# Kernel optimization log

Measured on AMD Instinct MI355X. Metric: run time of the kernel, lower is better.

The kernel has to match this reference:

```python
import jax, jax.numpy as jnp
import numpy as np

B, S, D, H = 2, 2048, 2048, 16
DK = D // H
THETA = 10000.0


def setup_inputs() -> dict:
    key = jax.random.key(0)
    ks = jax.random.split(key, 5)
    scale = 0.02
    return {
        "x": jax.random.normal(ks[0], (B, S, D), dtype=jnp.float32),
        "W_Q": jax.random.normal(ks[1], (D, D), dtype=jnp.float32) * scale,
        "W_K": jax.random.normal(ks[2], (D, D), dtype=jnp.float32) * scale,
        "W_V": jax.random.normal(ks[3], (D, D), dtype=jnp.float32) * scale,
        "W_O": jax.random.normal(ks[4], (D, D), dtype=jnp.float32) * scale,
        "token_positions": jnp.arange(S, dtype=jnp.int32),
    }


def _rope(x, pos):
    # x: [B, S, H, DK]; pos: [S]. Interleaved-pair rotation (cs336 RoPE).
    half = DK // 2
    inv_freq = THETA ** (-(jnp.arange(half, dtype=jnp.float32) / half))  # [half]
    ang = pos.astype(jnp.float32)[:, None] * inv_freq[None, :]           # [S, half]
    cos = jnp.cos(ang)[None, :, None, :]                                 # [1,S,1,half]
    sin = jnp.sin(ang)[None, :, None, :]
    x1, x2 = x[..., ::2], x[..., 1::2]
    r1 = x1 * cos - x2 * sin
    r2 = x1 * sin + x2 * cos
    return jnp.stack([r1, r2], axis=-1).reshape(x.shape)


def reference(x, W_Q, W_K, W_V, W_O, token_positions):
    # QKV projections (Linear with no bias: y = x @ W^T)
    Q = (x @ W_Q.T).reshape(B, S, H, DK)
    K = (x @ W_K.T).reshape(B, S, H, DK)
    V = (x @ W_V.T).reshape(B, S, H, DK)
    Q = _rope(Q, token_positions)
    K = _rope(K, token_positions)
    scores = jnp.einsum("bqhd,bkhd->bhqk", Q, K) / jnp.sqrt(jnp.float32(DK))
    causal = jnp.tril(jnp.ones((S, S), dtype=bool))  # True = attend
    scores = jnp.where(causal[None, None], scores, -jnp.inf)
    attn = jax.nn.softmax(scores, axis=-1)
    out = jnp.einsum("bhqk,bkhd->bqhd", attn, V).reshape(B, S, D)
    return out @ W_O.T
```

## Files before the change

kernel.cpp:

```cpp
#include <hip/hip_runtime.h>
#include <hip/hip_bf16.h>
#include <cstdint>
#include <cstddef>

#define B_ 2
#define S_ 2048
#define D_ 2048
#define H_ 16
#define DK_ 128
#define M_ (B_*S_)

typedef __attribute__((ext_vector_type(8))) __bf16 bf16x8;
typedef __attribute__((ext_vector_type(4))) float f32x4;
typedef __attribute__((ext_vector_type(16))) float f32x16;

__device__ __forceinline__ unsigned short f2bf(float f) {
  union { float f; unsigned int u; } v; v.f = f;
  unsigned int r = (v.u + 0x7fffu + ((v.u >> 16) & 1u)) >> 16;
  return (unsigned short)r;
}
__device__ __forceinline__ float bf2f(unsigned short b) {
  union { unsigned int u; float f; } v; v.u = ((unsigned int)b) << 16;
  return v.f;
}

__device__ __forceinline__ void gld16(const void* g, void* l) {
  __builtin_amdgcn_global_load_lds(
      (const __attribute__((address_space(1))) unsigned int*)g,
      (__attribute__((address_space(3))) unsigned int*)l, 16, 0, 0);
}

__global__ void cvt_all(const float* __restrict__ x,  const float* __restrict__ Wq,
                        const float* __restrict__ Wk, const float* __restrict__ Wv,
                        const float* __restrict__ Wo, unsigned short* __restrict__ dst) {
  size_t i = ((size_t)blockIdx.x * blockDim.x + threadIdx.x) * 4;
  const float* src;
  size_t off;
  if (i < ((size_t)M_ * D_)) {
    src = x; off = i;
  } else {
    size_t j = i - (size_t)M_ * D_;
    int w = (int)(j >> 22);
    off = j & ((1u << 22) - 1);
    src = (w == 0) ? Wq : (w == 1) ? Wk : (w == 2) ? Wv : Wo;
  }
  float4 v = *(const float4*)(src + off);
  dst[i+0] = f2bf(v.x); dst[i+1] = f2bf(v.y);
  dst[i+2] = f2bf(v.z); dst[i+3] = f2bf(v.w);
}

__global__ __launch_bounds__(512, 2) void gemm_qkv(const unsigned short* __restrict__ A,
                                                   const unsigned short* __restrict__ W0,
                                                   const unsigned short* __restrict__ W1,
                                                   const unsigned short* __restrict__ W2,
                                                   unsigned short* __restrict__ C0,
                                                   unsigned short* __restrict__ C1,
                                                   unsigned short* __restrict__ C2,
                                                   int M, int N, int K) {
  __shared__ unsigned short sA[2][2][256 * 32];
  __shared__ unsigned short sB[2][2][256 * 32];
  const int id   = blockIdx.x;
  const int tid  = threadIdx.x;
  const int lane = tid & 63;
  const int wid  = tid >> 6;
  const int l16 = lane & 15, quad = lane >> 4;
  const int col16 = quad ^ ((lane >> 1) & 3);
  const int qk_log = (lane & 3) ^ ((lane >> 3) & 3);
  const int srow = lane >> 2;
  const int NT = K >> 6;

  if (id < 256) {
    const int z = id >> 7, r = id & 127;
    const unsigned short* Bt = z ? W1 : W0;
    unsigned short* Cout = z ? C1 : C0;
    const int bm = (r >> 3) * 256, bn = (r & 7) * 256;
    const int wm = wid >> 2, wn = wid & 3;

    f32x4 acc[8][4];
    #pragma unroll
    for (int i = 0; i < 8; ++i)
      #pragma unroll
      for (int j = 0; j < 4; ++j)
        acc[i][j] = (f32x4){0.f, 0.f, 0.f, 0.f};

    auto stage = [&](const unsigned short* __restrict__ g, int rowbase,
                     unsigned short* l, int t, int kh) {
      const unsigned short* src = g + (size_t)rowbase * K + t * 64 + kh * 32 + qk_log * 8;
      #pragma unroll
      for (int p = 0; p < 2; ++p) {
        const int i = wid * 2 + p;
        gld16(src + (size_t)(i * 16 + srow) * K, l + i * 512);
      }
    };

    stage(A,  bm, &sA[0][0][0], 0, 0);
    stage(Bt, bn, &sB[0][0][0], 0, 0);
    stage(A,  bm, &sA[0][1][0], 0, 1);
    stage(Bt, bn, &sB[0][1][0], 0, 1);
    stage(A,  bm, &sA[1][0][0], 1, 0);
    stage(Bt, bn, &sB[1][0][0], 1, 0);
    asm volatile("s_waitcnt vmcnt(4)" ::: "memory");
    __builtin_amdgcn_s_barrier();

    for (int t = 0; t < NT; ++t) {
      const int buf = t & 1;
      bf16x8 bfrag[4];
      #pragma unroll
      for (int ph = 0; ph < 4; ++ph) {
        const int ks = ph >> 1;
        const int mh = ph & 1;
        bf16x8 afrag[4];
        const unsigned short* aP = &sA[buf][ks][0] +
            (size_t)((wm * 128 + mh * 64 + l16) * 4 + col16) * 8;
        #pragma unroll
        for (int mf = 0; mf < 4; ++mf)
          afrag[mf] = *(const bf16x8*)(aP + mf * 512);
        if (mh == 0) {
          const unsigned short* bP = &sB[buf][ks][0] +
              (size_t)((wn * 64 + l16) * 4 + col16) * 8;
          #pragma unroll
          for (int nf = 0; nf < 4; ++nf)
            bfrag[nf] = *(const bf16x8*)(bP + nf * 512);
        }
        if (ph == 0)      { if (t + 1 < NT) stage(A,  bm, &sA[buf ^ 1][1][0], t + 1, 1); }
        else if (ph == 1) { if (t + 1 < NT) stage(Bt, bn, &sB[buf ^ 1][1][0], t + 1, 1); }
        else if (ph == 2) { if (t + 2 < NT) stage(A,  bm, &sA[buf][0][0],     t + 2, 0); }
        else              { if (t + 2 < NT) stage(Bt, bn, &sB[buf][0][0],     t + 2, 0); }

        __builtin_amdgcn_s_barrier();
        asm volatile("s_waitcnt lgkmcnt(0)" ::: "memory");
        __builtin_amdgcn_s_setprio(1);
        #pragma unroll
        for (int nf = 0; nf < 4; ++nf)
          #pragma unroll
          for (int mf = 0; mf < 4; ++mf)
            acc[mh * 4 + mf][nf] = __builtin_amdgcn_mfma_f32_16x16x32_bf16(
                afrag[mf], bfrag[nf], acc[mh * 4 + mf][nf], 0, 0, 0);
        __builtin_amdgcn_s_setprio(0);
        if (ph == 3) {
          if (t + 2 < NT) asm volatile("s_waitcnt vmcnt(4)" ::: "memory");
          else            asm volatile("s_waitcnt vmcnt(0)" ::: "memory");
        }
        __builtin_amdgcn_s_barrier();
      }
    }

    #pragma unroll
    for (int mf = 0; mf < 8; ++mf) {
      const int row = bm + wm * 128 + mf * 16 + quad * 4;
      #pragma unroll
      for (int nf = 0; nf < 4; ++nf) {
        const int col = bn + wn * 64 + nf * 16 + l16;
        #pragma unroll
        for (int rr = 0; rr < 4; ++rr)
          Cout[(size_t)(row + rr) * N + col] = f2bf(acc[mf][nf][rr]);
      }
    }
  } else {
    const int r = id - 256;
    const unsigned short* Bt = W2;
    unsigned short* Cout = C2;
    const int bm = (r >> 3) * 128, bn = (r & 7) * 256;
    const int wm = wid >> 2, wn = wid & 3;

    f32x4 acc[4][4];
    #pragma unroll
    for (int i = 0; i < 4; ++i)
      #pragma unroll
      for (int j = 0; j < 4; ++j)
        acc[i][j] = (f32x4){0.f, 0.f, 0.f, 0.f};

    auto stageB = [&](unsigned short* l, int t, int kh) {
      const unsigned short* src = Bt + (size_t)bn * K + t * 64 + kh * 32 + qk_log * 8;
      #pragma unroll
      for (int p = 0; p < 2; ++p) {
        const int i = wid * 2 + p;
        gld16(src + (size_t)(i * 16 + srow) * K, l + i * 512);
      }
    };
    auto stageA = [&](unsigned short* l, int t, int kh) {
      const unsigned short* src = A + (size_t)bm * K + t * 64 + kh * 32 + qk_log * 8;
      gld16(src + (size_t)(wid * 16 + srow) * K, l + wid * 512);
    };

    stageA(&sA[0][0][0], 0, 0); stageB(&sB[0][0][0], 0, 0);
    stageA(&sA[0][1][0], 0, 1); stageB(&sB[0][1][0], 0, 1);
    stageA(&sA[1][0][0], 1, 0); stageB(&sB[1][0][0], 1, 0);
    asm volatile("s_waitcnt vmcnt(3)" ::: "memory");
    __builtin_amdgcn_s_barrier();

    for (int t = 0; t < NT; ++t) {
      const int buf = t & 1;
      #pragma unroll
      for (int ph = 0; ph < 2; ++ph) {
        bf16x8 afrag[4], bfrag[4];
        const unsigned short* aP = &sA[buf][ph][0] +
            (size_t)((wm * 64 + l16) * 4 + col16) * 8;
        #pragma unroll
        for (int mf = 0; mf < 4; ++mf)
          afrag[mf] = *(const bf16x8*)(aP + mf * 512);
        const unsigned short* bP = &sB[buf][ph][0] +
            (size_t)((wn * 64 + l16) * 4 + col16) * 8;
        #pragma unroll
        for (int nf = 0; nf < 4; ++nf)
          bfrag[nf] = *(const bf16x8*)(bP + nf * 512);

        if (ph == 0) { if (t + 1 < NT) { stageA(&sA[buf ^ 1][1][0], t + 1, 1);
                                         stageB(&sB[buf ^ 1][1][0], t + 1, 1); } }
        else         { if (t + 2 < NT) { stageA(&sA[buf][0][0], t + 2, 0);
                                         stageB(&sB[buf][0][0], t + 2, 0); } }

        __builtin_amdgcn_s_barrier();
        asm volatile("s_waitcnt lgkmcnt(0)" ::: "memory");
        __builtin_amdgcn_s_setprio(1);
        #pragma unroll
        for (int nf = 0; nf < 4; ++nf)
          #pragma unroll
          for (int mf = 0; mf < 4; ++mf)
            acc[mf][nf] = __builtin_amdgcn_mfma_f32_16x16x32_bf16(
                afrag[mf], bfrag[nf], acc[mf][nf], 0, 0, 0);
        __builtin_amdgcn_s_setprio(0);
        if (ph == 1) {
          if (t + 2 < NT) asm volatile("s_waitcnt vmcnt(3)" ::: "memory");
          else            asm volatile("s_waitcnt vmcnt(0)" ::: "memory");
        }
        __builtin_amdgcn_s_barrier();
      }
    }

    #pragma unroll
    for (int mf = 0; mf < 4; ++mf) {
      const int row = bm + wm * 64 + mf * 16 + quad * 4;
      #pragma unroll
      for (int nf = 0; nf < 4; ++nf) {
        const int col = bn + wn * 64 + nf * 16 + l16;
        #pragma unroll
        for (int rr = 0; rr < 4; ++rr)
          Cout[(size_t)(row + rr) * N + col] = f2bf(acc[mf][nf][rr]);
      }
    }
  }
}

template<int WRITE_BF16>
__global__ __launch_bounds__(256) void gemm_bt(const unsigned short* __restrict__ A,
                                               const unsigned short* __restrict__ W0,
                                               const unsigned short* __restrict__ W1,
                                               const unsigned short* __restrict__ W2,
                                               void* __restrict__ C0, void* __restrict__ C1,
                                               void* __restrict__ C2,
                                               int M, int N, int K) {
  __shared__ unsigned short sA[128 * 32];
  __shared__ unsigned short sB[128 * 32];
  const int z = blockIdx.z;
  const unsigned short* Bt = (z == 0) ? W0 : (z == 1) ? W1 : W2;
  void* Cout = (z == 0) ? C0 : (z == 1) ? C1 : C2;

  const int tid  = threadIdx.x;
  const int lane = tid & 63;
  const int wid  = tid >> 6;
  const int wm = wid >> 1, wn = wid & 1;
  const int quad = lane >> 4, l16 = lane & 15;
  const int bm = blockIdx.y * 128, bn = blockIdx.x * 128;
  const int srow = lane >> 2;
  const int scol = (lane & 3) * 8;

  f32x4 acc[4][4];
  #pragma unroll
  for (int i = 0; i < 4; ++i)
    #pragma unroll
    for (int j = 0; j < 4; ++j)
      acc[i][j] = (f32x4){0.f, 0.f, 0.f, 0.f};

  for (int k0 = 0; k0 < K; k0 += 32) {
    __syncthreads();
    #pragma unroll
    for (int p = 0; p < 2; ++p) {
      int row = p * 64 + wid * 16;
      gld16(A  + (size_t)(bm + row + srow) * K + k0 + scol, sA + row * 32);
      gld16(Bt + (size_t)(bn + row + srow) * K + k0 + scol, sB + row * 32);
    }
    __syncthreads();

    bf16x8 af[4], bfr[4];
    #pragma unroll
    for (int i = 0; i < 4; ++i)
      af[i] = *(const bf16x8*)(sA + (wm * 64 + i * 16 + l16) * 32 + quad * 8);
    #pragma unroll
    for (int j = 0; j < 4; ++j)
      bfr[j] = *(const bf16x8*)(sB + (wn * 64 + j * 16 + l16) * 32 + quad * 8);
    #pragma unroll
    for (int i = 0; i < 4; ++i)
      #pragma unroll
      for (int j = 0; j < 4; ++j)
        acc[i][j] = __builtin_amdgcn_mfma_f32_16x16x32_bf16(af[i], bfr[j], acc[i][j], 0, 0, 0);
  }

  #pragma unroll
  for (int i = 0; i < 4; ++i) {
    int row = bm + wm * 64 + i * 16 + quad * 4;
    #pragma unroll
    for (int j = 0; j < 4; ++j) {
      int col = bn + wn * 64 + j * 16 + l16;
      #pragma unroll
      for (int r = 0; r < 4; ++r) {
        if (WRITE_BF16)
          ((unsigned short*)Cout)[(size_t)(row + r) * N + col] = f2bf(acc[i][j][r]);
        else
          ((float*)Cout)[(size_t)(row + r) * N + col] = acc[i][j][r];
      }
    }
  }
}

__global__ void rope_kernel(unsigned short* __restrict__ Q, unsigned short* __restrict__ K,
                            const int* __restrict__ pos) {
  int idx = blockIdx.x * blockDim.x + threadIdx.x;
  int i = idx & 63;
  int h = (idx >> 6) & (H_ - 1);
  int s = (idx >> 10) & (S_ - 1);
  int b = idx >> 21;
  float p = (float)pos[s];
  float inv = __expf(-(float)i * (9.210340371976184f / 64.0f));
  float ang = p * inv;
  float sn, cs;
  __sincosf(ang, &sn, &cs);
  size_t base = (((size_t)b * S_ + s) * D_) + (size_t)h * DK_ + 2 * i;
  unsigned int q2 = *(const unsigned int*)(Q + base);
  float x1 = bf2f((unsigned short)(q2 & 0xffffu)), x2 = bf2f((unsigned short)(q2 >> 16));
  unsigned int lo = f2bf(x1 * cs - x2 * sn), hi = f2bf(x1 * sn + x2 * cs);
  *(unsigned int*)(Q + base) = lo | (hi << 16);
  unsigned int k2 = *(const unsigned int*)(K + base);
  x1 = bf2f((unsigned short)(k2 & 0xffffu)); x2 = bf2f((unsigned short)(k2 >> 16));
  lo = f2bf(x1 * cs - x2 * sn); hi = f2bf(x1 * sn + x2 * cs);
  *(unsigned int*)(K + base) = lo | (hi << 16);
}

__global__ __launch_bounds__(256) void transpose_bf16(const unsigned short* __restrict__ src,
                                                      unsigned short* __restrict__ dst) {
  __shared__ unsigned short sT[64 * 64];
  const int b = blockIdx.y;
  const int tx = blockIdx.x & 31, ty = blockIdx.x >> 5;
  const size_t base = (size_t)b * 2048 * 2048;
  const int m0 = ty * 64, c0 = tx * 64;
  const int tid = threadIdx.x;
  #pragma unroll
  for (int c = 0; c < 2; ++c) {
    int idx = tid + c * 256;
    int row = idx >> 3;
    int chk = idx & 7;
    uint4 v = *(const uint4*)(src + base + (size_t)(m0 + row) * 2048 + c0 + chk * 8);
    *(uint4*)(sT + row * 64 + ((chk ^ (row & 7)) * 8)) = v;
  }
  __syncthreads();
  #pragma unroll
  for (int c = 0; c < 2; ++c) {
    int idx = tid + c * 256;
    int orow = idx >> 3;
    int ocol = (idx & 7) * 8;
    unsigned short tmp[8];
    #pragma unroll
    for (int j = 0; j < 8; ++j) {
      int lr = ocol + j;
      int lc = orow;
      tmp[j] = sT[lr * 64 + (((lc >> 3) ^ (lr & 7)) * 8) + (lc & 7)];
    }
    *(uint4*)(dst + base + (size_t)(c0 + orow) * 2048 + m0 + ocol) = *(const uint4*)tmp;
  }
}

__global__ __launch_bounds__(256, 2) void flash_attn(const unsigned short* __restrict__ Q,
                                                     const unsigned short* __restrict__ K,
                                                     const unsigned short* __restrict__ VT,
                                                     unsigned short* __restrict__ O) {
  __shared__ unsigned short sK[2][64 * 128];
  __shared__ unsigned short sVT[2][128 * 64];
  __shared__ unsigned short sP[4][32 * 64];

  const int tid = threadIdx.x, lane = tid & 63, wid = tid >> 6;
  const int half = lane >> 5, l32 = lane & 31;
  const int qi = 15 - (blockIdx.x & 15);
  const int bh = blockIdx.x >> 4;
  const int h = bh & (H_ - 1), b = bh >> 4;
  const int qw = qi * 128 + wid * 32;
  const size_t qkbase = ((size_t)b * S_) * D_ + (size_t)h * DK_;
  const unsigned short* Qg = Q + qkbase;
  const unsigned short* Kg = K + qkbase;
  const unsigned short* VTg = VT + (size_t)bh * DK_ * S_;
  unsigned short* Og = O + qkbase;
  unsigned short* sPw = sP[wid];

  const int kKeySub = lane >> 4;
  const int kPhys   = lane & 15;
  const int vFeatSub = lane >> 3;
  const int vPhys    = lane & 7;

  bf16x8 qf[8];
  #pragma unroll
  for (int ks = 0; ks < 8; ++ks)
    qf[ks] = *(const bf16x8*)(Qg + (size_t)(qw + l32) * D_ + ks * 16 + half * 8);

  union { unsigned short u[8]; bf16x8 v; } onesu;
  #pragma unroll
  for (int j2 = 0; j2 < 8; ++j2) onesu.u[j2] = 0x3F80;
  const bf16x8 ones = onesu.v;

  f32x16 Oacc[4];
  #pragma unroll
  for (int ft = 0; ft < 4; ++ft)
    #pragma unroll
    for (int r = 0; r < 16; ++r) Oacc[ft][r] = 0.f;
  f32x16 l_acc;
  #pragma unroll
  for (int r = 0; r < 16; ++r) l_acc[r] = 0.f;
  const float scale = 0.08838834764831845f;

  const int nkb = 2 * (qi + 1);

  auto stage = [&](int kb) {
    const int k0 = kb * 64;
    unsigned short* bK = sK[kb & 1];
    unsigned short* bV = sVT[kb & 1];
    #pragma unroll
    for (int p = 0; p < 4; ++p) {
      int issue = wid * 4 + p;
      int key = issue * 4 + kKeySub;
      int logiK = (kPhys & 8) | ((kPhys ^ key) & 7);
      gld16(Kg + (size_t)(k0 + key) * D_ + logiK * 8, bK + issue * 512);
      int feat = issue * 8 + vFeatSub;
      int logiV = vPhys ^ (feat & 7);
      gld16(VTg + (size_t)feat * S_ + k0 + logiV * 8, bV + issue * 512);
    }
  };

  stage(0);

  for (int kb = 0; kb < nkb; ++kb) {
    __syncthreads();
    if (kb + 1 < nkb) stage(kb + 1);

    const int k0 = kb * 64;
    if (k0 > qw + 31) continue;

    const unsigned short* bK = sK[kb & 1];
    const unsigned short* bV = sVT[kb & 1];

    f32x16 sc[2];
    #pragma unroll
    for (int t = 0; t < 2; ++t)
      #pragma unroll
      for (int r = 0; r < 16; ++r) sc[t][r] = 0.f;
    __builtin_amdgcn_s_setprio(1);
    #pragma unroll
    for (int ks = 0; ks < 8; ++ks) {
      const int logi = ks * 2 + half;
      #pragma unroll
      for (int t = 0; t < 2; ++t) {
        const int key = t * 32 + l32;
        const int phys = (logi & 8) | ((logi ^ key) & 7);
        bf16x8 kf = *(const bf16x8*)(bK + key * 128 + phys * 8);
        sc[t] = __builtin_amdgcn_mfma_f32_32x32x16_bf16(qf[ks], kf, sc[t], 0, 0, 0);
      }
    }
    __builtin_amdgcn_s_setprio(0);

    const bool diag = (k0 + 63 > qw);
    #pragma unroll
    for (int t = 0; t < 2; ++t) {
      const int col = t * 32 + l32;
      const int keyg = k0 + col;
      #pragma unroll
      for (int r = 0; r < 16; ++r) {
        const int rl = (r & 3) + 8 * (r >> 2) + 4 * half;
        float v = sc[t][r] * scale;
        if (diag && (keyg > qw + rl)) v = -1e30f;
        sPw[rl * 64 + (((col >> 3) ^ (rl & 7)) * 8) + (col & 7)] = f2bf(__expf(v));
      }
    }

    __builtin_amdgcn_s_setprio(1);
    #pragma unroll
    for (int ksp = 0; ksp < 4; ++ksp) {
      const int logi = ksp * 2 + half;
      bf16x8 pf = *(const bf16x8*)(sPw + l32 * 64 + ((logi ^ (l32 & 7)) * 8));
      l_acc = __builtin_amdgcn_mfma_f32_32x32x16_bf16(pf, ones, l_acc, 0, 0, 0);
      #pragma unroll
      for (int ft = 0; ft < 4; ++ft) {
        const int feat = ft * 32 + l32;
        const int phys = logi ^ (feat & 7);
        bf16x8 vf = *(const bf16x8*)(bV + feat * 64 + phys * 8);
        Oacc[ft] = __builtin_amdgcn_mfma_f32_32x32x16_bf16(pf, vf, Oacc[ft], 0, 0, 0);
      }
    }
    __builtin_amdgcn_s_setprio(0);
  }

  #pragma unroll
  for (int ft = 0; ft < 4; ++ft) {
    const int feat = ft * 32 + l32;
    #pragma unroll
    for (int r = 0; r < 16; ++r) {
      const int rl = (r & 3) + 8 * (r >> 2) + 4 * half;
      Og[(size_t)(qw + rl) * D_ + feat] = f2bf(Oacc[ft][r] / l_acc[r]);
    }
  }
}

extern "C" void kernel_launch(void* const* d_in, const int* in_sizes, int n_in,
                              void* d_out, int out_size, void* d_ws, size_t ws_size,
                              hipStream_t stream) {
  const float* x  = (const float*)d_in[0];
  const float* Wq = (const float*)d_in[1];
  const float* Wk = (const float*)d_in[2];
  const float* Wv = (const float*)d_in[3];
  const float* Wo = (const float*)d_in[4];
  const int*  pos = (const int*)d_in[5];
  float* out = (float*)d_out;

  char* ws = (char*)d_ws;
  size_t off = 0;
  auto alloc = [&](size_t bytes) { void* p = ws + off; off += (bytes + 255) & ~255ULL; return p; };
  const size_t nx = (size_t)M_ * D_;
  const size_t nw = (size_t)D_ * D_;
  unsigned short* xb  = (unsigned short*)alloc(nx * 2);
  unsigned short* wqb = (unsigned short*)alloc(nw * 2);
  unsigned short* wkb = (unsigned short*)alloc(nw * 2);
  unsigned short* wvb = (unsigned short*)alloc(nw * 2);
  unsigned short* wob = (unsigned short*)alloc(nw * 2);
  unsigned short* Qb  = (unsigned short*)alloc(nx * 2);
  unsigned short* Kb  = (unsigned short*)alloc(nx * 2);
  unsigned short* Vb  = (unsigned short*)alloc(nx * 2);
  unsigned short* AOb = xb;
  unsigned short* VTb = wqb;

  hipLaunchKernelGGL(cvt_all, dim3((nx + 4 * nw) / 1024), dim3(256), 0, stream,
                     x, Wq, Wk, Wv, Wo, xb);

  hipLaunchKernelGGL(gemm_qkv, dim3(512), dim3(512), 0, stream,
                     xb, wqb, wkb, wvb, Qb, Kb, Vb, M_, D_, D_);

  hipLaunchKernelGGL(rope_kernel, dim3((B_ * S_ * H_ * 64) / 256), dim3(256), 0, stream, Qb, Kb, pos);

  hipLaunchKernelGGL(transpose_bf16, dim3(1024, 2), dim3(256), 0, stream, Vb, VTb);

  hipLaunchKernelGGL(flash_attn, dim3(B_ * H_ * (S_ / 128)), dim3(256), 0, stream, Qb, Kb, VTb, AOb);

  hipLaunchKernelGGL((gemm_bt<0>), dim3(D_ / 128, M_ / 128, 1), dim3(256), 0, stream,
                     AOb, wob, wob, wob, (void*)out, (void*)out, (void*)out, M_, D_, D_);
}
```

Before: 415.5 us.

## Replace output projection GEMM with pipelined double-buffered 256x128 tile kernel

Replaces the simple single-buffered output-projection GEMM with a 512-thread kernel using 256x128 tiles, double-buffered LDS with split K-halves, and async global-to-LDS prefetch issued ahead of the MFMA work. It adds an XOR-swizzled LDS layout to reduce bank conflicts and raises wave priority around the MFMA blocks. This is meant to hide global load latency and cut barrier stalls in the final projection. In exchange it uses more LDS per block and relies on hand-placed waitcnt counts, which must stay correct.

Measured after the change: 411.4 us. About the same (-1.0%).

```diff
diff --git a/kernel.cpp b/kernel.cpp
--- a/kernel.cpp
+++ b/kernel.cpp
@@ -242,28 +242,23 @@
   }
 }
 
-template<int WRITE_BF16>
-__global__ __launch_bounds__(256) void gemm_bt(const unsigned short* __restrict__ A,
-                                               const unsigned short* __restrict__ W0,
-                                               const unsigned short* __restrict__ W1,
-                                               const unsigned short* __restrict__ W2,
-                                               void* __restrict__ C0, void* __restrict__ C1,
-                                               void* __restrict__ C2,
-                                               int M, int N, int K) {
-  __shared__ unsigned short sA[128 * 32];
-  __shared__ unsigned short sB[128 * 32];
-  const int z = blockIdx.z;
-  const unsigned short* Bt = (z == 0) ? W0 : (z == 1) ? W1 : W2;
-  void* Cout = (z == 0) ? C0 : (z == 1) ? C1 : C2;
-
+__global__ __launch_bounds__(512, 2) void gemm_out(const unsigned short* __restrict__ A,
+                                                   const unsigned short* __restrict__ Bt,
+                                                   float* __restrict__ C,
+                                                   int M, int N, int K) {
+  __shared__ unsigned short sA[2][2][256 * 32];
+  __shared__ unsigned short sB[2][2][128 * 32];
+  const int id   = blockIdx.x;
   const int tid  = threadIdx.x;
   const int lane = tid & 63;
   const int wid  = tid >> 6;
+  const int l16 = lane & 15, quad = lane >> 4;
+  const int col16 = quad ^ ((lane >> 1) & 3);
+  const int qk_log = (lane & 3) ^ ((lane >> 3) & 3);
+  const int srow = lane >> 2;
+  const int NT = K >> 6;
+  const int bm = (id >> 4) * 256, bn = (id & 15) * 128;
   const int wm = wid >> 1, wn = wid & 1;
-  const int quad = lane >> 4, l16 = lane & 15;
-  const int bm = blockIdx.y * 128, bn = blockIdx.x * 128;
-  const int srow = lane >> 2;
-  const int scol = (lane & 3) * 8;
 
   f32x4 acc[4][4];
   #pragma unroll
@@ -272,43 +267,73 @@
     for (int j = 0; j < 4; ++j)
       acc[i][j] = (f32x4){0.f, 0.f, 0.f, 0.f};
 
-  for (int k0 = 0; k0 < K; k0 += 32) {
-    __syncthreads();
+  auto stageA = [&](unsigned short* l, int t, int kh) {
+    const unsigned short* src = A + (size_t)bm * K + t * 64 + kh * 32 + qk_log * 8;
     #pragma unroll
     for (int p = 0; p < 2; ++p) {
-      int row = p * 64 + wid * 16;
-      gld16(A  + (size_t)(bm + row + srow) * K + k0 + scol, sA + row * 32);
-      gld16(Bt + (size_t)(bn + row + srow) * K + k0 + scol, sB + row * 32);
-    }
-    __syncthreads();
-
-    bf16x8 af[4], bfr[4];
-    #pragma unroll
-    for (int i = 0; i < 4; ++i)
-      af[i] = *(const bf16x8*)(sA + (wm * 64 + i * 16 + l16) * 32 + quad * 8);
-    #pragma unroll
-    for (int j = 0; j < 4; ++j)
-      bfr[j] = *(const bf16x8*)(sB + (wn * 64 + j * 16 + l16) * 32 + quad * 8);
-    #pragma unroll
-    for (int i = 0; i < 4; ++i)
-      #pragma unroll
-      for (int j = 0; j < 4; ++j)
-        acc[i][j] = __builtin_amdgcn_mfma_f32_16x16x32_bf16(af[i], bfr[j], acc[i][j], 0, 0, 0);
-  }
-
-  #pragma unroll
-  for (int i = 0; i < 4; ++i) {
-    int row = bm + wm * 64 + i * 16 + quad * 4;
-    #pragma unroll
-    for (int j = 0; j < 4; ++j) {
-      int col = bn + wn * 64 + j * 16 + l16;
-      #pragma unroll
-      for (int r = 0; r < 4; ++r) {
-        if (WRITE_BF16)
-          ((unsigned short*)Cout)[(size_t)(row + r) * N + col] = f2bf(acc[i][j][r]);
-        else
-          ((float*)Cout)[(size_t)(row + r) * N + col] = acc[i][j][r];
-      }
+      const int i = wid * 2 + p;
+      gld16(src + (size_t)(i * 16 + srow) * K, l + i * 512);
+    }
+  };
+  auto stageB = [&](unsigned short* l, int t, int kh) {
+    const unsigned short* src = Bt + (size_t)bn * K + t * 64 + kh * 32 + qk_log * 8;
+    gld16(src + (size_t)(wid * 16 + srow) * K, l + wid * 512);
+  };
+
+  stageA(&sA[0][0][0], 0, 0); stageB(&sB[0][0][0], 0, 0);
+  stageA(&sA[0][1][0], 0, 1); stageB(&sB[0][1][0], 0, 1);
+  stageA(&sA[1][0][0], 1, 0); stageB(&sB[1][0][0], 1, 0);
+  asm volatile("s_waitcnt vmcnt(3)" ::: "memory");
+  __builtin_amdgcn_s_barrier();
+
+  for (int t = 0; t < NT; ++t) {
+    const int buf = t & 1;
+    #pragma unroll
+    for (int ph = 0; ph < 2; ++ph) {
+      bf16x8 afrag[4], bfrag[4];
+      const unsigned short* aP = &sA[buf][ph][0] +
+          (size_t)((wm * 64 + l16) * 4 + col16) * 8;
+      #pragma unroll
+      for (int mf = 0; mf < 4; ++mf)
+        afrag[mf] = *(const bf16x8*)(aP + mf * 512);
+      const unsigned short* bP = &sB[buf][ph][0] +
+          (size_t)((wn * 64 + l16) * 4 + col16) * 8;
+      #pragma unroll
+      for (int nf = 0; nf < 4; ++nf)
+        bfrag[nf] = *(const bf16x8*)(bP + nf * 512);
+
+      if (ph == 0) { if (t + 1 < NT) { stageA(&sA[buf ^ 1][1][0], t + 1, 1);
+                                       stageB(&sB[buf ^ 1][1][0], t + 1, 1); } }
+      else         { if (t + 2 < NT) { stageA(&sA[buf][0][0], t + 2, 0);
+                                       stageB(&sB[buf][0][0], t + 2, 0); } }
+
+      __builtin_amdgcn_s_barrier();
+      asm volatile("s_waitcnt lgkmcnt(0)" ::: "memory");
+      __builtin_amdgcn_s_setprio(1);
+      #pragma unroll
+      for (int nf = 0; nf < 4; ++nf)
+        #pragma unroll
+        for (int mf = 0; mf < 4; ++mf)
+          acc[mf][nf] = __builtin_amdgcn_mfma_f32_16x16x32_bf16(
+              afrag[mf], bfrag[nf], acc[mf][nf], 0, 0, 0);
+      __builtin_amdgcn_s_setprio(0);
+      if (ph == 1) {
+        if (t + 2 < NT) asm volatile("s_waitcnt vmcnt(3)" ::: "memory");
+        else            asm volatile("s_waitcnt vmcnt(0)" ::: "memory");
+      }
+      __builtin_amdgcn_s_barrier();
+    }
+  }
+
+  #pragma unroll
+  for (int mf = 0; mf < 4; ++mf) {
+    const int row = bm + wm * 64 + mf * 16 + quad * 4;
+    #pragma unroll
+    for (int nf = 0; nf < 4; ++nf) {
+      const int col = bn + wn * 64 + nf * 16 + l16;
+      #pragma unroll
+      for (int rr = 0; rr < 4; ++rr)
+        C[(size_t)(row + rr) * N + col] = acc[mf][nf][rr];
     }
   }
 }
@@ -545,6 +570,6 @@
 
   hipLaunchKernelGGL(flash_attn, dim3(B_ * H_ * (S_ / 128)), dim3(256), 0, stream, Qb, Kb, VTb, AOb);
 
-  hipLaunchKernelGGL((gemm_bt<0>), dim3(D_ / 128, M_ / 128, 1), dim3(256), 0, stream,
-                     AOb, wob, wob, wob, (void*)out, (void*)out, (void*)out, M_, D_, D_);
-}
+  hipLaunchKernelGGL(gemm_out, dim3((M_ / 256) * (D_ / 128)), dim3(512), 0, stream,
+                     AOb, wob, out, M_, D_, D_);
+}
```
